# Performance work log

Measured on AMD Instinct MI355X. Metric: run time of the kernel, lower is better.

The kernel has to match this reference:

```python
import jax, jax.numpy as jnp
import numpy as np

C, H, OUT = 64, 128, 64          # in_channels, hidden_dim, out_channels
N, E = 20000, 640000             # nodes, edges
LN_EPS = 1e-5


def layer_norm(x, g, b):
    mu = jnp.mean(x, axis=-1, keepdims=True)
    var = jnp.var(x, axis=-1, keepdims=True)
    return (x - mu) * jax.lax.rsqrt(var + LN_EPS) * g + b


def setup_inputs() -> dict:
    key = jax.random.key(0)
    ks = jax.random.split(key, 12)
    F = 2 * C + 5  # edge MLP input dim = 133

    def w(k, shape, fan_in):
        return jax.random.normal(k, shape, jnp.float32) / np.float32(np.sqrt(fan_in))

    return {
        "x": jax.random.normal(ks[0], (N, C), jnp.float32),
        "pos": jax.random.normal(ks[1], (N, 2), jnp.float32),
        "vel": jax.random.normal(ks[2], (N, 2), jnp.float32),
        # phi_e: Linear(F,H) -> LN -> Softplus -> Linear(H,H) -> Softplus -> Linear(H,H)
        "We1": w(ks[3], (F, H), F), "be1": jnp.zeros((H,), jnp.float32),
        "ge1": jnp.ones((H,), jnp.float32), "bte1": jnp.zeros((H,), jnp.float32),
        "We2": w(ks[4], (H, H), H), "be2": jnp.zeros((H,), jnp.float32),
        "We3": w(ks[5], (H, H), H), "be3": jnp.zeros((H,), jnp.float32),
        # phi_v: Linear(F,H) -> LN -> Softplus -> Linear(H,1)
        "Wv1": w(ks[6], (F, H), F), "bv1": jnp.zeros((H,), jnp.float32),
        "gv1": jnp.ones((H,), jnp.float32), "btv1": jnp.zeros((H,), jnp.float32),
        "Wv2": w(ks[7], (H, 1), H), "bv2": jnp.zeros((1,), jnp.float32),
        # phi_h: Linear(C+H+1,H) -> LN -> Softplus -> Linear(H,OUT)
        "Wh1": w(ks[8], (C + H + 1, H), C + H + 1), "bh1": jnp.zeros((H,), jnp.float32),
        "gh1": jnp.ones((H,), jnp.float32), "bth1": jnp.zeros((H,), jnp.float32),
        "Wh2": w(ks[9], (H, OUT), H), "bh2": jnp.zeros((OUT,), jnp.float32),
        "edge_index": jax.random.randint(ks[10], (2, E), 0, N, dtype=jnp.int64)
        if jax.config.jax_enable_x64 else jax.random.randint(ks[10], (2, E), 0, N, dtype=jnp.int32),
    }


def reference(x, pos, vel,
              We1, be1, ge1, bte1, We2, be2, We3, be3,
              Wv1, bv1, gv1, btv1, Wv2, bv2,
              Wh1, bh1, gh1, bth1, Wh2, bh2,
              edge_index):
    src = edge_index[0]  # j (source / x_j)
    dst = edge_index[1]  # i (target / x_i, aggregation index)

    # per-edge geometric features (gather)
    rel_pos = pos[src] - pos[dst]                                   # [E,2]
    rel_vel = vel[src] - vel[dst]                                   # [E,2]
    dist_sq = jnp.sum(rel_pos ** 2, axis=-1, keepdims=True)         # [E,1]
    dot_vr = jnp.sum(rel_vel * rel_pos, axis=-1, keepdims=True)     # [E,1]
    r2_inv = jnp.minimum(1.0 / (dist_sq + 0.05), 20.0)
    r6_inv = jnp.minimum(r2_inv ** 3, 400.0)
    r12_inv = jnp.minimum(r6_inv ** 2, 160000.0)

    tmp = jnp.concatenate([x[dst], x[src], dist_sq, dot_vr,
                           r2_inv, r6_inv, r12_inv], axis=1)        # [E, 2C+5]

    # phi_e (edge MLP)
    h = jax.nn.softplus(layer_norm(tmp @ We1 + be1, ge1, bte1))
    h = jax.nn.softplus(h @ We2 + be2)
    m_h_e = h @ We3 + be3                                           # [E,H]

    # phi_v (scalar weight on rel_pos -> equivariant vector message)
    v = jax.nn.softplus(layer_norm(tmp @ Wv1 + bv1, gv1, btv1))
    v_w = v @ Wv2 + bv2                                             # [E,1]
    m_v_e = v_w * rel_pos                                           # [E,2]

    # scatter-mean aggregation to target nodes
    n_nodes = x.shape[0]
    ones = jnp.ones((src.shape[0], 1), x.dtype)
    cnt = jax.ops.segment_sum(ones, dst, num_segments=n_nodes)
    denom = jnp.maximum(cnt, 1.0)
    m_h = jax.ops.segment_sum(m_h_e, dst, num_segments=n_nodes) / denom   # [N,H]
    m_v = jax.ops.segment_sum(m_v_e, dst, num_segments=n_nodes) / denom   # [N,2]

    m_v_norm = jnp.sqrt(jnp.sum((m_v + 1e-8) ** 2, axis=-1, keepdims=True))  # [N,1]

    # phi_h (node update MLP); shortcut is Identity since C == OUT
    hin = jnp.concatenate([x, m_h, m_v_norm], axis=-1)              # [N, C+H+1]
    hu = jax.nn.softplus(layer_norm(hin @ Wh1 + bh1, gh1, bth1))
    h_update = hu @ Wh2 + bh2                                       # [N,OUT]
    return x + h_update
```

## Files before the change

kernel.cpp:

```cpp
#include <hip/hip_runtime.h>
#include <stdint.h>

#define NCH    64
#define HID    128
#define OUTC   64
#define NNODE  20000
#define NEDGE  640000
#define FDIM   133
#define PHIN   193
#define TE     32
#define TN     32
#define NST    36
#define LN_EPS 1e-5f
#define KP1    160
#define KP2    128

typedef __attribute__((ext_vector_type(8))) short bf16x8;
typedef __attribute__((ext_vector_type(4))) float f32x4;

__device__ __forceinline__ unsigned short f2bf(float f) {
    union { float f; unsigned int i; } v; v.f = f;
    unsigned int b = v.i;
    return (unsigned short)((b + 0x7FFFu + ((b >> 16) & 1u)) >> 16);
}
__device__ __forceinline__ float sp(float xv) {
    return fmaxf(xv, 0.f) + __logf(1.0f + __expf(-fabsf(xv)));
}
__device__ __forceinline__ void atomAddF(float* p, float v) {
    __hip_atomic_fetch_add(p, v, __ATOMIC_RELAXED, __HIP_MEMORY_SCOPE_AGENT);
}
__device__ __forceinline__ int fragOff(int ks, int mt, int lanepos) {
    return ((ks * 2 + mt) * 64 + lanepos) * 8;
}

#define WS_WFLOAT (NNODE * HID + NNODE * 2 + NNODE)
#define WT_WE1 0
#define WT_WV1 (128 * KP1)
#define WT_WE2 (2 * 128 * KP1)
#define WT_WE3 (2 * 128 * KP1 + 128 * KP2)
#define WT_TOTAL (2 * 128 * KP1 + 2 * 128 * KP2)

__global__ __launch_bounds__(256)
void eg_prep(const float* __restrict__ We1, const float* __restrict__ Wv1,
             const float* __restrict__ We2, const float* __restrict__ We3,
             short* __restrict__ wt)
{
    int idx = blockIdx.x * 256 + threadIdx.x;
    if (idx >= WT_TOTAL) return;
    if (idx < WT_WV1) {
        int n = idx / KP1, k = idx % KP1;
        wt[idx] = (k < FDIM) ? (short)f2bf(We1[(size_t)k * HID + n]) : (short)0;
    } else if (idx < WT_WE2) {
        int r = idx - WT_WV1; int n = r / KP1, k = r % KP1;
        wt[idx] = (k < FDIM) ? (short)f2bf(Wv1[(size_t)k * HID + n]) : (short)0;
    } else if (idx < WT_WE3) {
        int r = idx - WT_WE2; int n = r / KP2, k = r % KP2;
        wt[idx] = (short)f2bf(We2[(size_t)k * HID + n]);
    } else {
        int r = idx - WT_WE3; int n = r / KP2, k = r % KP2;
        wt[idx] = (short)f2bf(We3[(size_t)k * HID + n]);
    }
}

__global__ __launch_bounds__(256, 6)
void eg_edge(const float* __restrict__ x, const float* __restrict__ pos,
             const float* __restrict__ vel,
             const float* __restrict__ be1, const float* __restrict__ ge1,
             const float* __restrict__ bte1, const float* __restrict__ be2,
             const float* __restrict__ be3,
             const float* __restrict__ bv1, const float* __restrict__ gv1,
             const float* __restrict__ btv1,
             const float* __restrict__ Wv2, const float* __restrict__ bv2,
             const short* __restrict__ wt,
             const int* __restrict__ ei,
             float* __restrict__ mh, float* __restrict__ mv,
             float* __restrict__ cnt)
{
    __shared__ __align__(16) short frag_s[5 * 2 * 64 * 8];
    __shared__ float psum_s[512];
    __shared__ float mu_s[64], rs_s[64];
    __shared__ int   dst_s[TE], src_s[TE];
    __shared__ float rel_s[TE * 2], vw_s[TE];

    const int tid  = threadIdx.x;
    const int lane = tid & 63;
    const int wid  = tid >> 6;
    const int lr   = lane & 15;
    const int quad = lane >> 4;
    const int n0w  = wid * 32;
    const int e_base = blockIdx.x * TE;

    const short* We1T = wt + WT_WE1;
    const short* Wv1T = wt + WT_WV1;
    const short* We2T = wt + WT_WE2;
    const short* We3T = wt + WT_WE3;

    float geo[5];
    if (tid < TE) {
        int gi = e_base + tid;
        int eS = ei[gi];
        int eD = ei[NEDGE + gi];
        src_s[tid] = eS; dst_s[tid] = eD;
        float rx = pos[2 * eS]     - pos[2 * eD];
        float ry = pos[2 * eS + 1] - pos[2 * eD + 1];
        float vx = vel[2 * eS]     - vel[2 * eD];
        float vy = vel[2 * eS + 1] - vel[2 * eD + 1];
        float dsq = rx * rx + ry * ry;
        float dvr = vx * rx + vy * ry;
        float r2  = fminf(1.0f / (dsq + 0.05f), 20.0f);
        float r6  = fminf(r2 * r2 * r2, 400.0f);
        float r12 = fminf(r6 * r6, 160000.0f);
        geo[0] = dsq; geo[1] = dvr; geo[2] = r2; geo[3] = r6; geo[4] = r12;
        rel_s[2 * tid] = rx; rel_s[2 * tid + 1] = ry;
    }
    if (tid < 128) {
        int4 z = {0, 0, 0, 0};
        *(int4*)&frag_s[4 * 2 * 64 * 8 + tid * 8] = z;
    }
    __syncthreads();

    if (tid < TE) {
        int off = fragOff(4, tid >> 4, (tid & 15));
        #pragma unroll
        for (int j = 0; j < 5; ++j) frag_s[off + j] = (short)f2bf(geo[j]);
    }
    {
        const int e = tid & 31, slot = tid >> 5;
        const int d = dst_s[e], s = src_s[e];
        #pragma unroll
        for (int h = 0; h < 2; ++h) {
            int o = slot + h * 8;
            int node = h ? s : d;
            int c0 = (o & 7) * 8;
            const float4 a0 = *(const float4*)&x[(size_t)node * NCH + c0];
            const float4 a1 = *(const float4*)&x[(size_t)node * NCH + c0 + 4];
            bf16x8 v;
            v[0] = (short)f2bf(a0.x); v[1] = (short)f2bf(a0.y);
            v[2] = (short)f2bf(a0.z); v[3] = (short)f2bf(a0.w);
            v[4] = (short)f2bf(a1.x); v[5] = (short)f2bf(a1.y);
            v[6] = (short)f2bf(a1.z); v[7] = (short)f2bf(a1.w);
            int ks = o >> 2, kq = o & 3;
            *(bf16x8*)&frag_s[fragOff(ks, e >> 4, kq * 16 + (e & 15))] = v;
        }
    }
    __syncthreads();

    const int ncol0 = n0w + lr;
    const int ncol1 = n0w + 16 + lr;

    f32x4 zero4 = {0.f, 0.f, 0.f, 0.f};
    f32x4 accE[2][2], accV[2][2];
    #pragma unroll
    for (int mt = 0; mt < 2; ++mt)
        #pragma unroll
        for (int nt = 0; nt < 2; ++nt) { accE[mt][nt] = zero4; accV[mt][nt] = zero4; }
    for (int ks = 0; ks < 5; ++ks) {
        bf16x8 af0 = *(const bf16x8*)&frag_s[fragOff(ks, 0, lane)];
        bf16x8 af1 = *(const bf16x8*)&frag_s[fragOff(ks, 1, lane)];
        int krow = ks * 32 + quad * 8;
        #pragma unroll
        for (int nt = 0; nt < 2; ++nt) {
            int n = n0w + nt * 16 + lr;
            bf16x8 bwE = *(const bf16x8*)&We1T[n * KP1 + krow];
            bf16x8 bwV = *(const bf16x8*)&Wv1T[n * KP1 + krow];
            accE[0][nt] = __builtin_amdgcn_mfma_f32_16x16x32_bf16(af0, bwE, accE[0][nt], 0, 0, 0);
            accE[1][nt] = __builtin_amdgcn_mfma_f32_16x16x32_bf16(af1, bwE, accE[1][nt], 0, 0, 0);
            accV[0][nt] = __builtin_amdgcn_mfma_f32_16x16x32_bf16(af0, bwV, accV[0][nt], 0, 0, 0);
            accV[1][nt] = __builtin_amdgcn_mfma_f32_16x16x32_bf16(af1, bwV, accV[1][nt], 0, 0, 0);
        }
    }
    {
        float be0 = be1[ncol0], be_1 = be1[ncol1];
        float bv0 = bv1[ncol0], bv_1 = bv1[ncol1];
        #pragma unroll
        for (int mt = 0; mt < 2; ++mt)
            #pragma unroll
            for (int r = 0; r < 4; ++r) {
                accE[mt][0][r] += be0; accE[mt][1][r] += be_1;
                accV[mt][0][r] += bv0; accV[mt][1][r] += bv_1;
            }
    }

    #pragma unroll
    for (int mt = 0; mt < 2; ++mt)
        #pragma unroll
        for (int r = 0; r < 4; ++r) {
            float se = accE[mt][0][r] + accE[mt][1][r];
            float qe = accE[mt][0][r] * accE[mt][0][r] + accE[mt][1][r] * accE[mt][1][r];
            float sv = accV[mt][0][r] + accV[mt][1][r];
            float qv = accV[mt][0][r] * accV[mt][0][r] + accV[mt][1][r] * accV[mt][1][r];
            #pragma unroll
            for (int m = 1; m < 16; m <<= 1) {
                se += __shfl_xor(se, m, 16);
                qe += __shfl_xor(qe, m, 16);
                sv += __shfl_xor(sv, m, 16);
                qv += __shfl_xor(qv, m, 16);
            }
            if (lr == 0) {
                int row = mt * 16 + quad * 4 + r;
                psum_s[      row * 4 + wid] = se;
                psum_s[128 + row * 4 + wid] = qe;
                psum_s[256 + row * 4 + wid] = sv;
                psum_s[384 + row * 4 + wid] = qv;
            }
        }
    __syncthreads();
    if (tid < 64) {
        int p = tid >> 5, row = tid & 31;
        float s = 0.f, q = 0.f;
        #pragma unroll
        for (int w = 0; w < 4; ++w) {
            s += psum_s[p * 256 +       row * 4 + w];
            q += psum_s[p * 256 + 128 + row * 4 + w];
        }
        float mu = s * (1.0f / HID);
        float var = q * (1.0f / HID) - mu * mu;
        mu_s[p * 32 + row] = mu;
        rs_s[p * 32 + row] = rsqrtf(var + LN_EPS);
    }
    __syncthreads();

    {
        float gE0 = ge1[ncol0], gE1 = ge1[ncol1];
        float tE0 = bte1[ncol0], tE1 = bte1[ncol1];
        float gV0 = gv1[ncol0], gV1 = gv1[ncol1];
        float tV0 = btv1[ncol0], tV1 = btv1[ncol1];
        float w20 = Wv2[ncol0], w21 = Wv2[ncol1];
        int ks0 = ncol0 >> 5, kq0 = (ncol0 & 31) >> 3, j0 = ncol0 & 7;
        int ks1 = ncol1 >> 5, kq1 = (ncol1 & 31) >> 3, j1 = ncol1 & 7;
        int fo0 = (ks0 * 128 + kq0 * 16) * 8 + j0;
        int fo1 = (ks1 * 128 + kq1 * 16) * 8 + j1;
        #pragma unroll
        for (int mt = 0; mt < 2; ++mt)
            #pragma unroll
            for (int r = 0; r < 4; ++r) {
                int rlow = quad * 4 + r, row = mt * 16 + rlow;
                float mu = mu_s[row], rsv = rs_s[row];
                float muV = mu_s[32 + row], rsV = rs_s[32 + row];
                float h0 = sp((accE[mt][0][r] - mu) * rsv * gE0 + tE0);
                float h1 = sp((accE[mt][1][r] - mu) * rsv * gE1 + tE1);
                frag_s[fo0 + (mt * 64 + rlow) * 8] = (short)f2bf(h0);
                frag_s[fo1 + (mt * 64 + rlow) * 8] = (short)f2bf(h1);
                float v0 = sp((accV[mt][0][r] - muV) * rsV * gV0 + tV0);
                float v1 = sp((accV[mt][1][r] - muV) * rsV * gV1 + tV1);
                float vp = v0 * w20 + v1 * w21;
                #pragma unroll
                for (int m = 1; m < 16; m <<= 1) vp += __shfl_xor(vp, m, 16);
                if (lr == 0) psum_s[row * 4 + wid] = vp;
            }
    }
    __syncthreads();
    if (tid < TE) {
        float s = 0.f;
        #pragma unroll
        for (int w = 0; w < 4; ++w) s += psum_s[tid * 4 + w];
        vw_s[tid] = s + bv2[0];
    }

    {
        f32x4 acc2[2][2];
        #pragma unroll
        for (int mt = 0; mt < 2; ++mt)
            #pragma unroll
            for (int nt = 0; nt < 2; ++nt) acc2[mt][nt] = zero4;
        for (int ks = 0; ks < 4; ++ks) {
            bf16x8 af0 = *(const bf16x8*)&frag_s[fragOff(ks, 0, lane)];
            bf16x8 af1 = *(const bf16x8*)&frag_s[fragOff(ks, 1, lane)];
            int krow = ks * 32 + quad * 8;
            #pragma unroll
            for (int nt = 0; nt < 2; ++nt) {
                int n = n0w + nt * 16 + lr;
                bf16x8 bw = *(const bf16x8*)&We2T[n * KP2 + krow];
                acc2[0][nt] = __builtin_amdgcn_mfma_f32_16x16x32_bf16(af0, bw, acc2[0][nt], 0, 0, 0);
                acc2[1][nt] = __builtin_amdgcn_mfma_f32_16x16x32_bf16(af1, bw, acc2[1][nt], 0, 0, 0);
            }
        }
        __syncthreads();
        #pragma unroll
        for (int nt = 0; nt < 2; ++nt) {
            int kg = n0w + nt * 16 + lr;
            float b2 = be2[kg];
            int ks = kg >> 5, kq = (kg & 31) >> 3, j = kg & 7;
            #pragma unroll
            for (int mt = 0; mt < 2; ++mt)
                #pragma unroll
                for (int r = 0; r < 4; ++r) {
                    short v = (short)f2bf(sp(acc2[mt][nt][r] + b2));
                    frag_s[fragOff(ks, mt, kq * 16 + quad * 4 + r) + j] = v;
                }
        }
    }
    __syncthreads();

    {
        f32x4 acc3[2][2];
        #pragma unroll
        for (int mt = 0; mt < 2; ++mt)
            #pragma unroll
            for (int nt = 0; nt < 2; ++nt) acc3[mt][nt] = zero4;
        for (int ks = 0; ks < 4; ++ks) {
            bf16x8 af0 = *(const bf16x8*)&frag_s[fragOff(ks, 0, lane)];
            bf16x8 af1 = *(const bf16x8*)&frag_s[fragOff(ks, 1, lane)];
            int krow = ks * 32 + quad * 8;
            #pragma unroll
            for (int nt = 0; nt < 2; ++nt) {
                int n = n0w + nt * 16 + lr;
                bf16x8 bw = *(const bf16x8*)&We3T[n * KP2 + krow];
                acc3[0][nt] = __builtin_amdgcn_mfma_f32_16x16x32_bf16(af0, bw, acc3[0][nt], 0, 0, 0);
                acc3[1][nt] = __builtin_amdgcn_mfma_f32_16x16x32_bf16(af1, bw, acc3[1][nt], 0, 0, 0);
            }
        }
        #pragma unroll
        for (int nt = 0; nt < 2; ++nt) {
            int n = n0w + nt * 16 + lr;
            float b3 = be3[n];
            #pragma unroll
            for (int mt = 0; mt < 2; ++mt)
                #pragma unroll
                for (int r = 0; r < 4; ++r) {
                    int m = mt * 16 + quad * 4 + r;
                    atomAddF(&mh[(size_t)dst_s[m] * HID + n], acc3[mt][nt][r] + b3);
                }
        }
    }
    if (tid < TE) {
        int d = dst_s[tid];
        float w = vw_s[tid];
        atomAddF(&mv[2 * d],     w * rel_s[2 * tid]);
        atomAddF(&mv[2 * d + 1], w * rel_s[2 * tid + 1]);
        atomAddF(&cnt[d], 1.0f);
    }
}

__global__ __launch_bounds__(256)
void eg_node(const float* __restrict__ x,
             const float* __restrict__ Wh1, const float* __restrict__ bh1,
             const float* __restrict__ gh1, const float* __restrict__ bth1,
             const float* __restrict__ Wh2, const float* __restrict__ bh2,
             const float* __restrict__ mh, const float* __restrict__ mv,
             const float* __restrict__ cnt, float* __restrict__ out)
{
    __shared__ float hin_s[PHIN * NST];
    __shared__ float H_s[HID * NST];
    __shared__ float den_s[TN], mu_s[TN], rs_s[TN];

    const int tid = threadIdx.x;
    const int n_base = blockIdx.x * TN;

    if (tid < TN) {
        int n = n_base + tid;
        float den = 1.f, norm = 0.f;
        if (n < NNODE) {
            den = fmaxf(cnt[n], 1.0f);
            float ax = mv[2 * n] / den + 1e-8f;
            float ay = mv[2 * n + 1] / den + 1e-8f;
            norm = sqrtf(ax * ax + ay * ay);
        }
        den_s[tid] = den;
        hin_s[192 * NST + tid] = norm;
    }
    __syncthreads();
    {
        const int c = tid & 63, ng = tid >> 6;
        #pragma unroll
        for (int it = 0; it < 8; ++it) {
            int nl = it * 4 + ng;
            int n = n_base + nl;
            hin_s[c * NST + nl] = (n < NNODE) ? x[(size_t)n * NCH + c] : 0.f;
        }
        const int k = tid & 127, ng2 = tid >> 7;
        #pragma unroll
        for (int it = 0; it < 16; ++it) {
            int nl = it * 2 + ng2;
            int n = n_base + nl;
            hin_s[(NCH + k) * NST + nl] =
                (n < NNODE) ? mh[(size_t)n * HID + k] / den_s[nl] : 0.f;
        }
    }
    __syncthreads();

    const int n0 = (tid & 7) * 4;
    const int j0 = (tid >> 3) * 4;

    {
        float acc[4][4] = {};
        for (int k = 0; k < PHIN; ++k) {
            const float4 a = *(const float4*)&hin_s[k * NST + n0];
            const float4 wb = *(const float4*)(Wh1 + (size_t)k * HID + j0);
            const float w[4] = { wb.x, wb.y, wb.z, wb.w };
            const float aa[4] = { a.x, a.y, a.z, a.w };
            #pragma unroll
            for (int i = 0; i < 4; ++i)
                #pragma unroll
                for (int j = 0; j < 4; ++j) acc[i][j] += aa[i] * w[j];
        }
        #pragma unroll
        for (int j = 0; j < 4; ++j) {
            float b = bh1[j0 + j];
            #pragma unroll
            for (int i = 0; i < 4; ++i)
                H_s[(j0 + j) * NST + n0 + i] = acc[i][j] + b;
        }
    }
    __syncthreads();

    if (tid < TN) {
        float sum = 0.f, sq = 0.f;
        for (int k = 0; k < HID; ++k) {
            float v = H_s[k * NST + tid];
            sum += v; sq += v * v;
        }
        float mu = sum * (1.0f / HID);
        float var = sq * (1.0f / HID) - mu * mu;
        mu_s[tid] = mu;
        rs_s[tid] = rsqrtf(var + LN_EPS);
    }
    __syncthreads();
    {
        const int nl = tid & 31;
        const int jb = (tid >> 5) * 16;
        const float mu = mu_s[nl], rs = rs_s[nl];
        for (int jj = 0; jj < 16; ++jj) {
            int j = jb + jj;
            float v = H_s[j * NST + nl];
            v = (v - mu) * rs * gh1[j] + bth1[j];
            H_s[j * NST + nl] = sp(v);
        }
    }
    __syncthreads();

    {
        const int o0 = (tid >> 3) * 2;
        float acc[4][2] = {};
        for (int k = 0; k < HID; ++k) {
            const float4 a = *(const float4*)&H_s[k * NST + n0];
            const float2 wb = *(const float2*)(Wh2 + (size_t)k * OUTC + o0);
            const float aa[4] = { a.x, a.y, a.z, a.w };
            #pragma unroll
            for (int i = 0; i < 4; ++i) {
                acc[i][0] += aa[i] * wb.x;
                acc[i][1] += aa[i] * wb.y;
            }
        }
        #pragma unroll
        for (int jo = 0; jo < 2; ++jo) {
            float bo = bh2[o0 + jo];
            #pragma unroll
            for (int i = 0; i < 4; ++i) {
                int n = n_base + n0 + i;
                if (n < NNODE) {
                    out[(size_t)n * OUTC + o0 + jo] =
                        x[(size_t)n * NCH + o0 + jo] + acc[i][jo] + bo;
                }
            }
        }
    }
}

extern "C" void kernel_launch(void* const* d_in, const int* in_sizes, int n_in,
                              void* d_out, int out_size, void* d_ws, size_t ws_size,
                              hipStream_t stream)
{
    const float* x    = (const float*)d_in[0];
    const float* pos  = (const float*)d_in[1];
    const float* vel  = (const float*)d_in[2];
    const float* We1  = (const float*)d_in[3];
    const float* be1  = (const float*)d_in[4];
    const float* ge1  = (const float*)d_in[5];
    const float* bte1 = (const float*)d_in[6];
    const float* We2  = (const float*)d_in[7];
    const float* be2  = (const float*)d_in[8];
    const float* We3  = (const float*)d_in[9];
    const float* be3  = (const float*)d_in[10];
    const float* Wv1  = (const float*)d_in[11];
    const float* bv1  = (const float*)d_in[12];
    const float* gv1  = (const float*)d_in[13];
    const float* btv1 = (const float*)d_in[14];
    const float* Wv2  = (const float*)d_in[15];
    const float* bv2  = (const float*)d_in[16];
    const float* Wh1  = (const float*)d_in[17];
    const float* bh1  = (const float*)d_in[18];
    const float* gh1  = (const float*)d_in[19];
    const float* bth1 = (const float*)d_in[20];
    const float* Wh2  = (const float*)d_in[21];
    const float* bh2  = (const float*)d_in[22];
    const int*   ei   = (const int*)d_in[23];

    float* mh  = (float*)d_ws;
    float* mv  = mh + (size_t)NNODE * HID;
    float* cnt = mv + (size_t)NNODE * 2;
    short* wt  = (short*)(((float*)d_ws) + WS_WFLOAT);

    size_t zbytes = (size_t)WS_WFLOAT * sizeof(float);
    hipMemsetAsync(d_ws, 0, zbytes, stream);

    eg_prep<<<dim3((WT_TOTAL + 255) / 256), dim3(256), 0, stream>>>(We1, Wv1, We2, We3, wt);

    eg_edge<<<dim3(NEDGE / TE), dim3(256), 0, stream>>>(
        x, pos, vel, be1, ge1, bte1, be2, be3,
        bv1, gv1, btv1, Wv2, bv2, wt, ei, mh, mv, cnt);

    eg_node<<<dim3((NNODE + TN - 1) / TN), dim3(256), 0, stream>>>(
        x, Wh1, bh1, gh1, bth1, Wh2, bh2, mh, mv, cnt, (float*)d_out);
}
```

Measured before the change: 618.4 us.

## Sort edges by destination and pre-reduce messages in shared memory before atomics

Adds a counting sort of edges by destination node, built from three kernels: a degree histogram, a single-block prefix scan and a scatter into a permutation array. The edge kernel processes edges in permuted order and writes its per-edge messages to a shared buffer. It then run-length reduces consecutive edges that share a destination before issuing float atomics, which should cut global atomic traffic on mh/mv by roughly the average degree of 32 per tile. In exchange it adds extra launches, a serial 1024-thread scan, more shared memory per block (occupancy hint lowered from 6 to 5) and a random gather through perm. Because atomic ordering varies, the summation order is still nondeterministic.

```diff
diff --git a/kernel.cpp b/kernel.cpp
--- a/kernel.cpp
+++ b/kernel.cpp
@@ -14,6 +14,7 @@
 #define LN_EPS 1e-5f
 #define KP1    160
 #define KP2    128
+#define CAG    132
 
 typedef __attribute__((ext_vector_type(8))) short bf16x8;
 typedef __attribute__((ext_vector_type(4))) float f32x4;
@@ -33,7 +34,6 @@
     return ((ks * 2 + mt) * 64 + lanepos) * 8;
 }
 
-#define WS_WFLOAT (NNODE * HID + NNODE * 2 + NNODE)
 #define WT_WE1 0
 #define WT_WV1 (128 * KP1)
 #define WT_WE2 (2 * 128 * KP1)
@@ -62,7 +62,49 @@
     }
 }
 
-__global__ __launch_bounds__(256, 6)
+__global__ __launch_bounds__(256)
+void eg_hist(const int* __restrict__ ei, int* __restrict__ deg)
+{
+    int i = blockIdx.x * 256 + threadIdx.x;
+    if (i < NEDGE)
+        __hip_atomic_fetch_add(&deg[ei[NEDGE + i]], 1, __ATOMIC_RELAXED, __HIP_MEMORY_SCOPE_AGENT);
+}
+
+__global__ __launch_bounds__(1024)
+void eg_scan(const int* __restrict__ deg, int* __restrict__ cur)
+{
+    __shared__ int part[1024];
+    const int tid = threadIdx.x;
+    const int chunk = (NNODE + 1023) / 1024;
+    const int base = tid * chunk;
+    const int lim = min(base + chunk, NNODE);
+    int s = 0;
+    for (int j = base; j < lim; ++j) s += deg[j];
+    part[tid] = s;
+    __syncthreads();
+    for (int off = 1; off < 1024; off <<= 1) {
+        int v = (tid >= off) ? part[tid - off] : 0;
+        __syncthreads();
+        part[tid] += v;
+        __syncthreads();
+    }
+    int run = (tid > 0) ? part[tid - 1] : 0;
+    for (int j = base; j < lim; ++j) { cur[j] = run; run += deg[j]; }
+}
+
+__global__ __launch_bounds__(256)
+void eg_scatter(const int* __restrict__ ei, int* __restrict__ cur,
+                int* __restrict__ perm)
+{
+    int i = blockIdx.x * 256 + threadIdx.x;
+    if (i < NEDGE) {
+        int d = ei[NEDGE + i];
+        int p = __hip_atomic_fetch_add(&cur[d], 1, __ATOMIC_RELAXED, __HIP_MEMORY_SCOPE_AGENT);
+        perm[p] = i;
+    }
+}
+
+__global__ __launch_bounds__(256, 5)
 void eg_edge(const float* __restrict__ x, const float* __restrict__ pos,
              const float* __restrict__ vel,
              const float* __restrict__ be1, const float* __restrict__ ge1,
@@ -72,11 +114,11 @@
              const float* __restrict__ btv1,
              const float* __restrict__ Wv2, const float* __restrict__ bv2,
              const short* __restrict__ wt,
-             const int* __restrict__ ei,
-             float* __restrict__ mh, float* __restrict__ mv,
-             float* __restrict__ cnt)
+             const int* __restrict__ ei, const int* __restrict__ perm,
+             float* __restrict__ mh, float* __restrict__ mv)
 {
     __shared__ __align__(16) short frag_s[5 * 2 * 64 * 8];
+    __shared__ __align__(16) float cagg_s[TE * CAG];
     __shared__ float psum_s[512];
     __shared__ float mu_s[64], rs_s[64];
     __shared__ int   dst_s[TE], src_s[TE];
@@ -97,7 +139,7 @@
 
     float geo[5];
     if (tid < TE) {
-        int gi = e_base + tid;
+        int gi = perm[e_base + tid];
         int eS = ei[gi];
         int eD = ei[NEDGE + gi];
         src_s[tid] = eS; dst_s[tid] = eD;
@@ -319,16 +361,37 @@
                 #pragma unroll
                 for (int r = 0; r < 4; ++r) {
                     int m = mt * 16 + quad * 4 + r;
-                    atomAddF(&mh[(size_t)dst_s[m] * HID + n], acc3[mt][nt][r] + b3);
+                    cagg_s[m * CAG + n] = acc3[mt][nt][r] + b3;
                 }
         }
     }
-    if (tid < TE) {
-        int d = dst_s[tid];
-        float w = vw_s[tid];
-        atomAddF(&mv[2 * d],     w * rel_s[2 * tid]);
-        atomAddF(&mv[2 * d + 1], w * rel_s[2 * tid + 1]);
-        atomAddF(&cnt[d], 1.0f);
+    __syncthreads();
+
+    {
+        const int c = tid & 127, h = tid >> 7;
+        const int m0 = h * 16;
+        float run = cagg_s[m0 * CAG + c];
+        int curd = dst_s[m0];
+        #pragma unroll
+        for (int m = m0 + 1; m < m0 + 16; ++m) {
+            int d = dst_s[m];
+            float v = cagg_s[m * CAG + c];
+            if (d == curd) run += v;
+            else { atomAddF(&mh[(size_t)curd * HID + c], run); curd = d; run = v; }
+        }
+        atomAddF(&mh[(size_t)curd * HID + c], run);
+    }
+    if (tid < 2) {
+        const int c = tid;
+        float run = vw_s[0] * rel_s[c];
+        int curd = dst_s[0];
+        for (int m = 1; m < TE; ++m) {
+            int d = dst_s[m];
+            float v = vw_s[m] * rel_s[2 * m + c];
+            if (d == curd) run += v;
+            else { atomAddF(&mv[2 * curd + c], run); curd = d; run = v; }
+        }
+        atomAddF(&mv[2 * curd + c], run);
     }
 }
 
@@ -338,7 +401,7 @@
              const float* __restrict__ gh1, const float* __restrict__ bth1,
              const float* __restrict__ Wh2, const float* __restrict__ bh2,
              const float* __restrict__ mh, const float* __restrict__ mv,
-             const float* __restrict__ cnt, float* __restrict__ out)
+             const int* __restrict__ deg, float* __restrict__ out)
 {
     __shared__ float hin_s[PHIN * NST];
     __shared__ float H_s[HID * NST];
@@ -351,7 +414,7 @@
         int n = n_base + tid;
         float den = 1.f, norm = 0.f;
         if (n < NNODE) {
-            den = fmaxf(cnt[n], 1.0f);
+            den = fmaxf((float)deg[n], 1.0f);
             float ax = mv[2 * n] / den + 1e-8f;
             float ay = mv[2 * n + 1] / den + 1e-8f;
             norm = sqrtf(ax * ax + ay * ay);
@@ -486,20 +549,25 @@
     const float* bh2  = (const float*)d_in[22];
     const int*   ei   = (const int*)d_in[23];
 
-    float* mh  = (float*)d_ws;
-    float* mv  = mh + (size_t)NNODE * HID;
-    float* cnt = mv + (size_t)NNODE * 2;
-    short* wt  = (short*)(((float*)d_ws) + WS_WFLOAT);
-
-    size_t zbytes = (size_t)WS_WFLOAT * sizeof(float);
+    float* mh   = (float*)d_ws;
+    float* mv   = mh + (size_t)NNODE * HID;
+    int*   deg  = (int*)(mv + NNODE * 2);
+    int*   cur  = deg + NNODE;
+    int*   perm = cur + NNODE;
+    short* wt   = (short*)(perm + NEDGE);
+
+    size_t zbytes = ((size_t)NNODE * HID + NNODE * 2 + NNODE) * sizeof(float);
     hipMemsetAsync(d_ws, 0, zbytes, stream);
 
     eg_prep<<<dim3((WT_TOTAL + 255) / 256), dim3(256), 0, stream>>>(We1, Wv1, We2, We3, wt);
+    eg_hist<<<dim3(NEDGE / 256), dim3(256), 0, stream>>>(ei, deg);
+    eg_scan<<<dim3(1), dim3(1024), 0, stream>>>(deg, cur);
+    eg_scatter<<<dim3(NEDGE / 256), dim3(256), 0, stream>>>(ei, cur, perm);
 
     eg_edge<<<dim3(NEDGE / TE), dim3(256), 0, stream>>>(
         x, pos, vel, be1, ge1, bte1, be2, be3,
-        bv1, gv1, btv1, Wv2, bv2, wt, ei, mh, mv, cnt);
+        bv1, gv1, btv1, Wv2, bv2, wt, ei, perm, mh, mv);
 
     eg_node<<<dim3((NNODE + TN - 1) / TN), dim3(256), 0, stream>>>(
-        x, Wh1, bh1, gh1, bth1, Wh2, bh2, mh, mv, cnt, (float*)d_out);
-}
+        x, Wh1, bh1, gh1, bth1, Wh2, bh2, mh, mv, deg, (float*)d_out);
+}
```

Measured after the change: 598.5 us. -3.2%, faster.
